# Kernel optimization log

Hardware: AMD Instinct MI355X
Metric: run time of the kernel (lower is better)

Reference implementation:

```python
import jax, jax.numpy as jnp
import numpy as np

B, T, D, H, C = 8, 1024, 1024, 16, 8  # batch, seq, d_model, heads, num_concepts
DK = D // H
LAMBD = 5.0


def setup_inputs() -> dict:
    key = jax.random.key(0)
    ks = jax.random.split(key, 14)
    s = 0.02
    return {
        "qa_concept": jax.random.normal(ks[0], (B, T, T, C), jnp.float32),
        "query": jax.random.normal(ks[1], (B, T, D), jnp.float32),
        "key": jax.random.normal(ks[2], (B, T, D), jnp.float32),
        "value": jax.random.normal(ks[3], (B, T, D), jnp.float32),
        "Wq": jax.random.normal(ks[4], (D, D), jnp.float32) * s,
        "bq": jnp.zeros((D,), jnp.float32),
        "Wk": jax.random.normal(ks[5], (D, D), jnp.float32) * s,
        "bk": jnp.zeros((D,), jnp.float32),
        "Wv": jax.random.normal(ks[6], (D, D), jnp.float32) * s,
        "bv": jnp.zeros((D,), jnp.float32),
        "Wo": jax.random.normal(ks[7], (D, D), jnp.float32) * s,
        "bo": jnp.zeros((D,), jnp.float32),
        "mask": jax.random.randint(ks[8], (B, T), 0, 2, jnp.int32),
    }


def reference(qa_concept, query, key, value, Wq, bq, Wk, bk, Wv, bv, Wo, bo, mask):
    # Linear projections (torch Linear: y = x @ W.T + b)
    q = (query @ Wq.T + bq).reshape(B, T, H, DK).transpose(0, 2, 1, 3)  # [B,H,T,dk]
    k = (key @ Wk.T + bk).reshape(B, T, H, DK).transpose(0, 2, 1, 3)
    v = (value @ Wv.T + bv).reshape(B, T, H, DK).transpose(0, 2, 1, 3)
    scores = jnp.einsum("bhqd,bhkd->bhqk", q, k) / jnp.sqrt(jnp.float32(DK))
    # concept bias added to first C heads only
    bias = LAMBD * jnp.transpose(qa_concept, (0, 3, 1, 2))  # [B,C,T,T]
    scores = scores.at[:, :C, :, :].add(bias)
    # mask: [B,T] -> [B,1,1,T], fill -1e9 where 0
    scores = jnp.where(mask[:, None, None, :] == 0, jnp.float32(-1e9), scores)
    attn = jax.nn.softmax(scores, axis=-1)  # dropout is identity in eval
    x = jnp.einsum("bhqk,bhkd->bhqd", attn, v)
    x = x.transpose(0, 2, 1, 3).reshape(B, T, D)
    return x @ Wo.T + bo
```

## Files before the change

### kernel.cpp

```cpp
#include <hip/hip_runtime.h>

#define B_  8
#define T_  1024
#define D_  1024
#define H_  16
#define DK_ 64
#define C_  8
#define N_  (B_*T_)

typedef __attribute__((ext_vector_type(8))) short bf16x8;
typedef __attribute__((ext_vector_type(4))) float f32x4;
typedef __attribute__((ext_vector_type(8))) unsigned short u16x8;
typedef __attribute__((ext_vector_type(4))) unsigned short u16x4;

__device__ __forceinline__ float bf2f(unsigned short u) {
  union { unsigned int i; float f; } x; x.i = ((unsigned int)u) << 16; return x.f;
}
__device__ __forceinline__ unsigned short f2bf(float f) {
  union { float f; unsigned int i; } x; x.f = f;
  unsigned int r = (x.i + 0x7fffu + ((x.i >> 16) & 1u)) >> 16;
  return (unsigned short)r;
}
__device__ __forceinline__ unsigned short f2h(float f) {
  union { _Float16 h; unsigned short u; } x; x.h = (_Float16)f; return x.u;
}
__device__ __forceinline__ float h2f(unsigned short u) {
  union { _Float16 h; unsigned short u; } x; x.u = u; return (float)x.h;
}

__device__ __forceinline__ void gl_lds16(const unsigned short* g, unsigned short* l) {
  __builtin_amdgcn_global_load_lds(
      (const __attribute__((address_space(1))) unsigned int*)g,
      (__attribute__((address_space(3))) unsigned int*)l,
      16, 0, 0);
}

__global__ __launch_bounds__(256) void cvt_qkv(
    const float* __restrict__ q, const float* __restrict__ k,
    const float* __restrict__ v, unsigned short* __restrict__ qo,
    unsigned short* __restrict__ ko, unsigned short* __restrict__ vo, int n4) {
  int seg = blockIdx.x >> 10;
  int bid = blockIdx.x & 1023;
  const float* in = (seg == 0) ? q : (seg == 1) ? k : v;
  unsigned short* out = (seg == 0) ? qo : (seg == 1) ? ko : vo;
  int tid = bid * blockDim.x + threadIdx.x;
  int stride = 1024 * 256;
  const float4* in4 = (const float4*)in;
  u16x4* out4 = (u16x4*)out;
  for (int i = tid; i < n4; i += stride) {
    float4 vv = in4[i];
    u16x4 o = { f2bf(vv.x), f2bf(vv.y), f2bf(vv.z), f2bf(vv.w) };
    out4[i] = o;
  }
}

__global__ __launch_bounds__(256) void cvt_w(
    const float* __restrict__ w0, const float* __restrict__ w1,
    const float* __restrict__ w2, const float* __restrict__ w3,
    unsigned short* __restrict__ o0, unsigned short* __restrict__ o1,
    unsigned short* __restrict__ o2, unsigned short* __restrict__ o3, int n4) {
  int seg = blockIdx.x >> 8;
  int bid = blockIdx.x & 255;
  const float* in = (seg == 0) ? w0 : (seg == 1) ? w1 : (seg == 2) ? w2 : w3;
  unsigned short* out = (seg == 0) ? o0 : (seg == 1) ? o1 : (seg == 2) ? o2 : o3;
  int tid = bid * blockDim.x + threadIdx.x;
  int stride = 256 * 256;
  const float4* in4 = (const float4*)in;
  u16x4* out4 = (u16x4*)out;
  for (int i = tid; i < n4; i += stride) {
    float4 vv = in4[i];
    u16x4 o = { f2bf(vv.x), f2bf(vv.y), f2bf(vv.z), f2bf(vv.w) };
    out4[i] = o;
  }
}

__global__ __launch_bounds__(256) void transposeQa(
    const float* __restrict__ qa, unsigned short* __restrict__ qat) {
  int b = blockIdx.x >> 10, q = blockIdx.x & 1023;
  int t = threadIdx.x;
  __shared__ float L[8][132];
  const float* src = qa + ((size_t)(b*T_ + q))*T_*C_;
  for (int ch = 0; ch < 8; ++ch) {
    int k0 = ch*128;
    float4 v = *(const float4*)(src + (size_t)(k0 + (t>>1))*C_ + (t&1)*4);
    int c4 = (t&1)*4, kk = t>>1;
    L[c4+0][kk] = v.x; L[c4+1][kk] = v.y; L[c4+2][kk] = v.z; L[c4+3][kk] = v.w;
    __syncthreads();
    int c = t >> 5, kk2 = (t&31)*4;
    float4 p = *(const float4*)&L[c][kk2];
    u16x4 o = { f2h(p.x), f2h(p.y), f2h(p.z), f2h(p.w) };
    *(u16x4*)(qat + ((size_t)(b*C_ + c)*T_ + q)*T_ + k0 + kk2) = o;
    __syncthreads();
  }
}

__global__ __launch_bounds__(256) void transposeV(
    const unsigned short* __restrict__ V, unsigned short* __restrict__ Vt) {
  int bid = blockIdx.x;
  int tt = bid & 15;
  int bh = bid >> 4;
  int b = bh >> 4, h = bh & 15;
  __shared__ unsigned short L[64][72];
  int r  = threadIdx.x >> 3;
  int c8 = (threadIdx.x & 7) * 8;
  const unsigned short* src = V + ((size_t)(b*T_ + tt*64))*D_ + h*64;
#pragma unroll
  for (int p = 0; p < 2; ++p) {
    int rr = r + p*32;
    u16x8 v = *(const u16x8*)(src + (size_t)rr*D_ + c8);
    *(u16x8*)&L[rr][c8] = v;
  }
  __syncthreads();
  unsigned short* dst = Vt + ((size_t)bh*64)*T_ + tt*64;
#pragma unroll
  for (int p = 0; p < 2; ++p) {
    int d = r + p*32;
    u16x8 o;
#pragma unroll
    for (int i = 0; i < 8; ++i) o[i] = L[c8 + i][d];
    *(u16x8*)(dst + (size_t)d*T_ + c8) = o;
  }
}

template <bool OUT_F32>
__device__ __forceinline__ void gemm_body(
    int blockid, const unsigned short* __restrict__ X,
    const unsigned short* __restrict__ W, const float* __restrict__ bias,
    void* __restrict__ Yv, unsigned short* As, unsigned short* Bs) {
  int orig = (blockid & 7) * 64 + (blockid >> 3);
  int bm = orig >> 3, bn = orig & 7;
  int t = threadIdx.x, lane = t & 63, w = t >> 6;
  int wr = w >> 1, wc = w & 1;
  int r16 = lane & 15, kg = lane >> 4;

  int srow0 = lane >> 2;
  int scol  = (lane & 3) * 8;
  const unsigned short* Ab = X + (size_t)(bm*128)*D_ + scol;
  const unsigned short* Bb = W + (size_t)(bn*128)*D_ + scol;

  f32x4 acc[4][4];
#pragma unroll
  for (int m = 0; m < 4; ++m)
#pragma unroll
    for (int n = 0; n < 4; ++n) acc[m][n] = (f32x4){0.f,0.f,0.f,0.f};

  for (int k0 = 0; k0 < D_; k0 += 32) {
    __syncthreads();
#pragma unroll
    for (int c = 0; c < 2; ++c) {
      int cidx = w*2 + c;
      int row = cidx*16 + srow0;
      gl_lds16(Ab + (size_t)row*D_ + k0, As + cidx*512);
      gl_lds16(Bb + (size_t)row*D_ + k0, Bs + cidx*512);
    }
    __syncthreads();

    bf16x8 a[4], bb[4];
#pragma unroll
    for (int m = 0; m < 4; ++m)
      a[m] = *(const bf16x8*)(As + (wr*64 + m*16 + r16)*32 + kg*8);
#pragma unroll
    for (int n = 0; n < 4; ++n)
      bb[n] = *(const bf16x8*)(Bs + (wc*64 + n*16 + r16)*32 + kg*8);
#pragma unroll
    for (int m = 0; m < 4; ++m)
#pragma unroll
      for (int n = 0; n < 4; ++n)
        acc[m][n] = __builtin_amdgcn_mfma_f32_16x16x32_bf16(a[m], bb[n], acc[m][n], 0, 0, 0);
  }

#pragma unroll
  for (int n = 0; n < 4; ++n) {
    int col = bn*128 + wc*64 + n*16 + r16;
    float bv = bias[col];
#pragma unroll
    for (int m = 0; m < 4; ++m) {
      int row0 = bm*128 + wr*64 + m*16 + kg*4;
#pragma unroll
      for (int jj = 0; jj < 4; ++jj) {
        float rv = acc[m][n][jj] + bv;
        if constexpr (OUT_F32)
          ((float*)Yv)[(size_t)(row0 + jj)*D_ + col] = rv;
        else
          ((unsigned short*)Yv)[(size_t)(row0 + jj)*D_ + col] = f2bf(rv);
      }
    }
  }
}

template <bool OUT_F32>
__global__ __launch_bounds__(256) void gemm_lds(
    const unsigned short* __restrict__ X, const unsigned short* __restrict__ W,
    const float* __restrict__ bias, void* __restrict__ Yv) {
  __shared__ __align__(16) unsigned short As[128*32];
  __shared__ __align__(16) unsigned short Bs[128*32];
  gemm_body<OUT_F32>(blockIdx.x, X, W, bias, Yv, As, Bs);
}

__global__ __launch_bounds__(256) void gemm_qkv(
    const unsigned short* __restrict__ Xq, const unsigned short* __restrict__ Xk,
    const unsigned short* __restrict__ Xv,
    const unsigned short* __restrict__ Wq2, const unsigned short* __restrict__ Wk2,
    const unsigned short* __restrict__ Wv2,
    const float* __restrict__ bq2, const float* __restrict__ bk2,
    const float* __restrict__ bv2,
    unsigned short* __restrict__ Yq, unsigned short* __restrict__ Yk,
    unsigned short* __restrict__ Yv2) {
  __shared__ __align__(16) unsigned short As[128*32];
  __shared__ __align__(16) unsigned short Bs[128*32];
  int seg = blockIdx.x >> 9, inner = blockIdx.x & 511;
  const unsigned short* X = (seg == 0) ? Xq : (seg == 1) ? Xk : Xv;
  const unsigned short* W = (seg == 0) ? Wq2 : (seg == 1) ? Wk2 : Wv2;
  const float* bias = (seg == 0) ? bq2 : (seg == 1) ? bk2 : bv2;
  unsigned short* Y = (seg == 0) ? Yq : (seg == 1) ? Yk : Yv2;
  gemm_body<false>(inner, X, W, bias, Y, As, Bs);
}

__global__ __launch_bounds__(256, 3) void attn4b(
    const unsigned short* __restrict__ Q, const unsigned short* __restrict__ K,
    const unsigned short* __restrict__ Vt, const unsigned short* __restrict__ qat,
    const int* __restrict__ mask, unsigned short* __restrict__ X) {
  int swzid = ((blockIdx.x & 7) << 7) | (blockIdx.x >> 3);
  int qt = swzid & 7, h = (swzid >> 3) & 15, b = swzid >> 7;
  int w = threadIdx.x >> 6, lane = threadIdx.x & 63;
  int r16 = lane & 15, kg = lane >> 4;
  int q0w = qt*128 + w*32;
  int bh = b*H_ + h;

  __shared__ unsigned short Ks[2][64][64];
  __shared__ unsigned short Vs[2][64][64];
  __shared__ unsigned int  P32[4][2][16][32];

  int rl = lane >> 3;
  int eo = ((lane & 7) * 8) ^ (rl << 3);
  const unsigned short* Kb = K + ((size_t)b*T_)*D_ + h*DK_;
  const unsigned short* Vb = Vt + ((size_t)bh*DK_)*T_;

  int sw16 = (r16 & 7) << 4;
  int ko0 = ((kg*16 +  0) ^ sw16) >> 1;
  int ko1 = ((kg*16 + 64) ^ sw16) >> 1;
  int sw32 = (r16 & 7) << 2;

  bf16x8 qfr[2][2];
#pragma unroll
  for (int qf = 0; qf < 2; ++qf) {
    const unsigned short* qrow = Q + ((size_t)b*T_ + q0w + qf*16 + r16)*D_ + h*DK_ + kg*8;
    qfr[qf][0] = *(const bf16x8*)qrow;
    qfr[qf][1] = *(const bf16x8*)(qrow + 32);
  }

  f32x4 acc[2][4];
#pragma unroll
  for (int qf = 0; qf < 2; ++qf)
#pragma unroll
    for (int db = 0; db < 4; ++db) acc[qf][db] = (f32x4){0.f,0.f,0.f,0.f};
  float mold[2] = {-3e38f, -3e38f};
  float lpart[2] = {0.f, 0.f};

  const int* mrow = mask + b*T_;
  const unsigned short* qab0 = qat + ((size_t)((b*C_ + h)*T_) + q0w + r16)*T_;

#pragma unroll
  for (int c = 0; c < 2; ++c) {
    int cc = w*2 + c;
    gl_lds16(Kb + (size_t)(cc*8 + rl)*D_ + eo, &Ks[0][cc*8][0]);
    gl_lds16(Vb + (size_t)(cc*8 + rl)*T_ + eo, &Vs[0][cc*8][0]);
  }
  __syncthreads();

  for (int t = 0; t < 16; ++t) {
    int k0 = t*64, bb = t & 1;
    if (t < 15) {
      int kn = k0 + 64, nb = bb ^ 1;
#pragma unroll
      for (int c = 0; c < 2; ++c) {
        int cc = w*2 + c;
        gl_lds16(Kb + (size_t)(kn + cc*8 + rl)*D_ + eo, &Ks[nb][cc*8][0]);
        gl_lds16(Vb + (size_t)(cc*8 + rl)*T_ + kn + eo, &Vs[nb][cc*8][0]);
      }
    }
    u16x4 qv[2][4];
    if (h < C_) {
#pragma unroll
      for (int qf = 0; qf < 2; ++qf)
#pragma unroll
        for (int kt = 0; kt < 4; ++kt)
          qv[qf][kt] = *(const u16x4*)(qab0 + (size_t)qf*16*T_ + k0 + kt*16 + kg*4);
    }
    int mk = mrow[k0 + lane];
    unsigned long long bits = __ballot(mk != 0);

    f32x4 s[2][4];
#pragma unroll
    for (int kt = 0; kt < 4; ++kt) {
      bf16x8 kf0 = *(const bf16x8*)&Ks[bb][kt*16 + r16][ko0];
      bf16x8 kf1 = *(const bf16x8*)&Ks[bb][kt*16 + r16][ko1];
#pragma unroll
      for (int qf = 0; qf < 2; ++qf) {
        f32x4 z = (f32x4){0.f,0.f,0.f,0.f};
        z = __builtin_amdgcn_mfma_f32_16x16x32_bf16(kf0, qfr[qf][0], z, 0, 0, 0);
        z = __builtin_amdgcn_mfma_f32_16x16x32_bf16(kf1, qfr[qf][1], z, 0, 0, 0);
        s[qf][kt] = z;
      }
    }

    float pmaxq[2];
#pragma unroll
    for (int qf = 0; qf < 2; ++qf) {
      float pmax = -3e38f;
#pragma unroll
      for (int kt = 0; kt < 4; ++kt)
#pragma unroll
        for (int jj = 0; jj < 4; ++jj) {
          float v = s[qf][kt][jj] * 0.125f;
          if (h < C_) v += 5.0f * h2f(qv[qf][kt][jj]);
          int idx = kt*16 + kg*4 + jj;
          v = ((bits >> idx) & 1ULL) ? v : -1e9f;
          s[qf][kt][jj] = v;
          pmax = fmaxf(pmax, v);
        }
      pmax = fmaxf(pmax, __shfl_xor(pmax, 16, 64));
      pmax = fmaxf(pmax, __shfl_xor(pmax, 32, 64));
      pmaxq[qf] = pmax;
    }
    if (!__all(pmaxq[0] - mold[0] <= 8.0f && pmaxq[1] - mold[1] <= 8.0f)) {
#pragma unroll
      for (int qf = 0; qf < 2; ++qf) {
        float mnew = fmaxf(mold[qf], pmaxq[qf]);
        float sc = __expf(mold[qf] - mnew);
        mold[qf] = mnew;
        lpart[qf] *= sc;
        float scq[4];
#pragma unroll
        for (int jj = 0; jj < 4; ++jj) scq[jj] = __shfl(sc, kg*4 + jj, 64);
#pragma unroll
        for (int db = 0; db < 4; ++db)
#pragma unroll
          for (int jj = 0; jj < 4; ++jj) acc[qf][db][jj] *= scq[jj];
      }
    }
#pragma unroll
    for (int qf = 0; qf < 2; ++qf) {
      unsigned int pk[8];
#pragma unroll
      for (int kt = 0; kt < 4; ++kt) {
        float p0 = __expf(s[qf][kt][0] - mold[qf]), p1 = __expf(s[qf][kt][1] - mold[qf]);
        float p2 = __expf(s[qf][kt][2] - mold[qf]), p3 = __expf(s[qf][kt][3] - mold[qf]);
        lpart[qf] += (p0 + p1) + (p2 + p3);
        pk[kt*2+0] = (unsigned)f2bf(p0) | ((unsigned)f2bf(p1) << 16);
        pk[kt*2+1] = (unsigned)f2bf(p2) | ((unsigned)f2bf(p3) << 16);
      }
#pragma unroll
      for (int kt = 0; kt < 4; ++kt)
        *(uint2*)&P32[w][qf][r16][(kt*8 + kg*2) ^ sw32] =
            make_uint2(pk[kt*2], pk[kt*2+1]);
    }
    __builtin_amdgcn_sched_barrier(0);
    asm volatile("s_waitcnt lgkmcnt(0)");
    __builtin_amdgcn_sched_barrier(0);
#pragma unroll
    for (int qf = 0; qf < 2; ++qf) {
      bf16x8 pa0 = *(const bf16x8*)&P32[w][qf][r16][(kg*4) ^ sw32];
      bf16x8 pa1 = *(const bf16x8*)&P32[w][qf][r16][(16 + kg*4) ^ sw32];
#pragma unroll
      for (int db = 0; db < 4; ++db) {
        bf16x8 vf0 = *(const bf16x8*)&Vs[bb][db*16 + r16][ko0];
        bf16x8 vf1 = *(const bf16x8*)&Vs[bb][db*16 + r16][ko1];
        acc[qf][db] = __builtin_amdgcn_mfma_f32_16x16x32_bf16(pa0, vf0, acc[qf][db], 0, 0, 0);
        acc[qf][db] = __builtin_amdgcn_mfma_f32_16x16x32_bf16(pa1, vf1, acc[qf][db], 0, 0, 0);
      }
    }
    __syncthreads();
  }

#pragma unroll
  for (int qf = 0; qf < 2; ++qf) {
    float lp = lpart[qf];
    lp += __shfl_xor(lp, 16, 64);
    lp += __shfl_xor(lp, 32, 64);
    float linv = 1.0f / lp;
    float invq[4];
#pragma unroll
    for (int jj = 0; jj < 4; ++jj) invq[jj] = __shfl(linv, kg*4 + jj, 64);
#pragma unroll
    for (int jj = 0; jj < 4; ++jj)
#pragma unroll
      for (int db = 0; db < 4; ++db)
        X[((size_t)b*T_ + q0w + qf*16 + kg*4 + jj)*D_ + h*DK_ + db*16 + r16] =
            f2bf(acc[qf][db][jj] * invq[jj]);
  }
}

__global__ __launch_bounds__(256) void attn_fused(
    const unsigned short* __restrict__ Q, const unsigned short* __restrict__ K,
    const unsigned short* __restrict__ Vt, const float* __restrict__ qa,
    const int* __restrict__ mask, unsigned short* __restrict__ X) {
  int bid = blockIdx.x;
  int qt = bid & 15, h = (bid >> 4) & 15, b = bid >> 8;
  int w = threadIdx.x >> 6, lane = threadIdx.x & 63;
  int r16 = lane & 15, kg = lane >> 4;
  int q0 = qt*64 + w*16;
  int bh = b*H_ + h;

  __shared__ unsigned short P[4][16][72];

  const unsigned short* qrow = Q + ((size_t)b*T_ + q0 + r16)*D_ + h*DK_ + kg*8;
  bf16x8 qf0 = *(const bf16x8*)qrow;
  bf16x8 qf1 = *(const bf16x8*)(qrow + 32);

  f32x4 acc[4];
#pragma unroll
  for (int db = 0; db < 4; ++db) acc[db] = (f32x4){0.f,0.f,0.f,0.f};
  float mrow[4], lrow[4];
#pragma unroll
  for (int jj = 0; jj < 4; ++jj) { mrow[jj] = -3e38f; lrow[jj] = 0.f; }

  const int* mptr = mask + b*T_;
  const unsigned short* Kbase = K + ((size_t)b*T_)*D_ + h*DK_;
  const unsigned short* Vbase = Vt + ((size_t)bh*DK_)*T_;
  const float* qabase = qa + ((size_t)(b*T_ + q0 + kg*4))*T_*C_ + h;

  for (int k0 = 0; k0 < T_; k0 += 64) {
    f32x4 s[4];
#pragma unroll
    for (int kt = 0; kt < 4; ++kt) {
      const unsigned short* krow = Kbase + (size_t)(k0 + kt*16 + r16)*D_ + kg*8;
      f32x4 z = (f32x4){0.f,0.f,0.f,0.f};
      z = __builtin_amdgcn_mfma_f32_16x16x32_bf16(qf0, *(const bf16x8*)krow,        z, 0, 0, 0);
      z = __builtin_amdgcn_mfma_f32_16x16x32_bf16(qf1, *(const bf16x8*)(krow + 32), z, 0, 0, 0);
      s[kt] = z;
    }
    int mk[4];
#pragma unroll
    for (int kt = 0; kt < 4; ++kt) mk[kt] = mptr[k0 + kt*16 + r16];
    if (h < C_) {
#pragma unroll
      for (int kt = 0; kt < 4; ++kt)
#pragma unroll
        for (int jj = 0; jj < 4; ++jj) {
          float bb = qabase[(size_t)jj*T_*C_ + (size_t)(k0 + kt*16 + r16)*C_];
          s[kt][jj] = s[kt][jj]*0.125f + 5.0f*bb;
        }
    } else {
#pragma unroll
      for (int kt = 0; kt < 4; ++kt)
#pragma unroll
        for (int jj = 0; jj < 4; ++jj) s[kt][jj] *= 0.125f;
    }
#pragma unroll
    for (int kt = 0; kt < 4; ++kt)
#pragma unroll
      for (int jj = 0; jj < 4; ++jj)
        if (mk[kt] == 0) s[kt][jj] = -1e9f;

#pragma unroll
    for (int jj = 0; jj < 4; ++jj) {
      float v = fmaxf(fmaxf(s[0][jj], s[1][jj]), fmaxf(s[2][jj], s[3][jj]));
#pragma unroll
      for (int d = 1; d < 16; d <<= 1) v = fmaxf(v, __shfl_xor(v, d, 64));
      float mnew = fmaxf(mrow[jj], v);
      float sc = __expf(mrow[jj] - mnew);
      mrow[jj] = mnew;
      lrow[jj] *= sc;
#pragma unroll
      for (int db = 0; db < 4; ++db) acc[db][jj] *= sc;
      float rs = 0.f;
#pragma unroll
      for (int kt = 0; kt < 4; ++kt) {
        float p = __expf(s[kt][jj] - mnew);
        rs += p;
        P[w][kg*4 + jj][kt*16 + r16] = f2bf(p);
      }
#pragma unroll
      for (int d = 1; d < 16; d <<= 1) rs += __shfl_xor(rs, d, 64);
      lrow[jj] += rs;
    }
    __syncthreads();

    bf16x8 pa0 = *(const bf16x8*)&P[w][r16][kg*8];
    bf16x8 pa1 = *(const bf16x8*)&P[w][r16][32 + kg*8];
#pragma unroll
    for (int db = 0; db < 4; ++db) {
      const unsigned short* vr = Vbase + (size_t)(db*16 + r16)*T_ + k0 + kg*8;
      acc[db] = __builtin_amdgcn_mfma_f32_16x16x32_bf16(pa0, *(const bf16x8*)vr,        acc[db], 0, 0, 0);
      acc[db] = __builtin_amdgcn_mfma_f32_16x16x32_bf16(pa1, *(const bf16x8*)(vr + 32), acc[db], 0, 0, 0);
    }
  }

  float inv[4];
#pragma unroll
  for (int jj = 0; jj < 4; ++jj) inv[jj] = 1.0f / lrow[jj];
#pragma unroll
  for (int jj = 0; jj < 4; ++jj)
#pragma unroll
    for (int db = 0; db < 4; ++db)
      X[((size_t)b*T_ + q0 + kg*4 + jj)*D_ + h*DK_ + db*16 + r16] =
          f2bf(acc[db][jj] * inv[jj]);
}

extern "C" void kernel_launch(void* const* d_in, const int* in_sizes, int n_in,
                              void* d_out, int out_size, void* d_ws, size_t ws_size,
                              hipStream_t stream) {
  const float* qa    = (const float*)d_in[0];
  const float* query = (const float*)d_in[1];
  const float* key   = (const float*)d_in[2];
  const float* value = (const float*)d_in[3];
  const float* Wq = (const float*)d_in[4];
  const float* bq = (const float*)d_in[5];
  const float* Wk = (const float*)d_in[6];
  const float* bk = (const float*)d_in[7];
  const float* Wv = (const float*)d_in[8];
  const float* bv = (const float*)d_in[9];
  const float* Wo = (const float*)d_in[10];
  const float* bo = (const float*)d_in[11];
  const int* mask = (const int*)d_in[12];

  const size_t ND = (size_t)N_ * D_;
  const size_t DD = (size_t)D_ * D_;
  const size_t QAT = (size_t)B_ * C_ * T_ * T_;
  unsigned short* Qws = (unsigned short*)d_ws;
  unsigned short* Kws = Qws + ND;
  unsigned short* Vws = Kws + ND;
  unsigned short* Xws = Vws + ND;
  unsigned short* qbf = Xws + ND;
  unsigned short* kbf = qbf + ND;
  unsigned short* vbf = kbf + ND;
  unsigned short* wqbf = vbf + ND;
  unsigned short* wkbf = wqbf + DD;
  unsigned short* wvbf = wkbf + DD;
  unsigned short* wobf = wvbf + DD;
  unsigned short* qatws = wobf + DD;
  unsigned short* Vtws = qbf;

  bool fast = ws_size >= (7*ND + 4*DD + QAT) * sizeof(unsigned short);

  dim3 blk(256);
  cvt_qkv<<<3072, blk, 0, stream>>>(query, key, value, qbf, kbf, vbf, (int)(ND/4));
  cvt_w<<<1024, blk, 0, stream>>>(Wq, Wk, Wv, Wo, wqbf, wkbf, wvbf, wobf, (int)(DD/4));

  gemm_qkv<<<3*512, blk, 0, stream>>>(qbf, kbf, vbf, wqbf, wkbf, wvbf,
                                      bq, bk, bv, Qws, Kws, Vws);

  transposeV<<<B_*H_*(T_/64), blk, 0, stream>>>(Vws, Vtws);

  if (fast) {
    transposeQa<<<B_*T_, blk, 0, stream>>>(qa, qatws);
    attn4b<<<B_*H_*(T_/128), blk, 0, stream>>>(Qws, Kws, Vtws, qatws, mask, Xws);
  } else {
    attn_fused<<<B_*H_*(T_/64), blk, 0, stream>>>(Qws, Kws, Vtws, qa, mask, Xws);
  }

  gemm_lds<true><<<512, blk, 0, stream>>>(Xws, wobf, bo, (float*)d_out);
}
```

Baseline: 324.2 us.

## Fuse QKV GEMM and qa_concept transpose into one interleaved kernel launch

Merges the compute-bound QKV projection GEMM and the memory-bound qa_concept transpose into one launch. Blocks are interleaved 3 GEMM tiles per 16 transpose blocks so both kinds run concurrently on the CUs and overlap compute with HBM traffic. The two paths share one 16KB shared buffer, and the separate transposeQa launch is removed. The risk is that the mixed blocks fight over resources, and the GEMM's occupancy is now set by the shared kernel's register and LDS use.

Result: slower. 391.4 us (+20.7%).

```diff
diff --git a/kernel.cpp b/kernel.cpp
--- a/kernel.cpp
+++ b/kernel.cpp
@@ -74,11 +74,11 @@
   }
 }
 
-__global__ __launch_bounds__(256) void transposeQa(
-    const float* __restrict__ qa, unsigned short* __restrict__ qat) {
-  int b = blockIdx.x >> 10, q = blockIdx.x & 1023;
+__device__ __forceinline__ void tqa_body(
+    int bid, const float* __restrict__ qa, unsigned short* __restrict__ qat,
+    float (*L)[132]) {
+  int b = bid >> 10, q = bid & 1023;
   int t = threadIdx.x;
-  __shared__ float L[8][132];
   const float* src = qa + ((size_t)(b*T_ + q))*T_*C_;
   for (int ch = 0; ch < 8; ++ch) {
     int k0 = ch*128;
@@ -92,6 +92,12 @@
     *(u16x4*)(qat + ((size_t)(b*C_ + c)*T_ + q)*T_ + k0 + kk2) = o;
     __syncthreads();
   }
+}
+
+__global__ __launch_bounds__(256) void transposeQa(
+    const float* __restrict__ qa, unsigned short* __restrict__ qat) {
+  __shared__ float L[8][132];
+  tqa_body(blockIdx.x, qa, qat, L);
 }
 
 __global__ __launch_bounds__(256) void transposeV(
@@ -216,6 +222,34 @@
   gemm_body<false>(inner, X, W, bias, Y, As, Bs);
 }
 
+__global__ __launch_bounds__(256) void gemm_qkv_tqa(
+    const unsigned short* __restrict__ Xq, const unsigned short* __restrict__ Xk,
+    const unsigned short* __restrict__ Xv,
+    const unsigned short* __restrict__ Wq2, const unsigned short* __restrict__ Wk2,
+    const unsigned short* __restrict__ Wv2,
+    const float* __restrict__ bq2, const float* __restrict__ bk2,
+    const float* __restrict__ bv2,
+    unsigned short* __restrict__ Yq, unsigned short* __restrict__ Yk,
+    unsigned short* __restrict__ Yv2,
+    const float* __restrict__ qa, unsigned short* __restrict__ qat) {
+  __shared__ __align__(16) unsigned char smem[16384];
+  int grp = blockIdx.x / 19;
+  int pos = blockIdx.x - grp*19;
+  if (pos < 3) {
+    int gid = grp*3 + pos;
+    int seg = gid >> 9, inner = gid & 511;
+    const unsigned short* X = (seg == 0) ? Xq : (seg == 1) ? Xk : Xv;
+    const unsigned short* W = (seg == 0) ? Wq2 : (seg == 1) ? Wk2 : Wv2;
+    const float* bias = (seg == 0) ? bq2 : (seg == 1) ? bk2 : bv2;
+    unsigned short* Y = (seg == 0) ? Yq : (seg == 1) ? Yk : Yv2;
+    unsigned short* As = (unsigned short*)smem;
+    gemm_body<false>(inner, X, W, bias, Y, As, As + 128*32);
+  } else {
+    int tid = grp*16 + (pos - 3);
+    tqa_body(tid, qa, qat, (float(*)[132])smem);
+  }
+}
+
 __global__ __launch_bounds__(256, 3) void attn4b(
     const unsigned short* __restrict__ Q, const unsigned short* __restrict__ K,
     const unsigned short* __restrict__ Vt, const unsigned short* __restrict__ qat,
@@ -538,15 +572,16 @@
   cvt_qkv<<<3072, blk, 0, stream>>>(query, key, value, qbf, kbf, vbf, (int)(ND/4));
   cvt_w<<<1024, blk, 0, stream>>>(Wq, Wk, Wv, Wo, wqbf, wkbf, wvbf, wobf, (int)(DD/4));
 
-  gemm_qkv<<<3*512, blk, 0, stream>>>(qbf, kbf, vbf, wqbf, wkbf, wvbf,
-                                      bq, bk, bv, Qws, Kws, Vws);
-
-  transposeV<<<B_*H_*(T_/64), blk, 0, stream>>>(Vws, Vtws);
-
   if (fast) {
-    transposeQa<<<B_*T_, blk, 0, stream>>>(qa, qatws);
+    gemm_qkv_tqa<<<19*512, blk, 0, stream>>>(qbf, kbf, vbf, wqbf, wkbf, wvbf,
+                                             bq, bk, bv, Qws, Kws, Vws,
+                                             qa, qatws);
+    transposeV<<<B_*H_*(T_/64), blk, 0, stream>>>(Vws, Vtws);
     attn4b<<<B_*H_*(T_/128), blk, 0, stream>>>(Qws, Kws, Vtws, qatws, mask, Xws);
   } else {
+    gemm_qkv<<<3*512, blk, 0, stream>>>(qbf, kbf, vbf, wqbf, wkbf, wvbf,
+                                        bq, bk, bv, Qws, Kws, Vws);
+    transposeV<<<B_*H_*(T_/64), blk, 0, stream>>>(Vws, Vtws);
     attn_fused<<<B_*H_*(T_/64), blk, 0, stream>>>(Qws, Kws, Vtws, qa, mask, Xws);
   }
 
```
